# Kernel tuning notes

Hardware: AMD Instinct MI355X
Metric: run time of the kernel (lower is better)

## Reference

```python
import jax, jax.numpy as jnp
import numpy as np
import math

D_MODEL = 256
NUM_HEADS = 8
D_HEAD = 32
K_EIG = 32
NUM_BANDS = 3


def setup_inputs() -> dict:
    key = jax.random.key(0)
    ks = jax.random.split(key, 12)
    B, N = 2, 50000
    x = jax.random.normal(ks[0], (B, N, D_MODEL), dtype=jnp.float32)
    eigenvectors = jax.random.normal(ks[1], (N, K_EIG), dtype=jnp.float32) / np.sqrt(N)
    eigenvalues = jnp.sort(jax.random.uniform(ks[2], (K_EIG,), dtype=jnp.float32))
    s = 1.0 / np.sqrt(D_MODEL)
    Wq = jax.random.normal(ks[3], (NUM_HEADS * D_HEAD, D_MODEL), dtype=jnp.float32) * s
    bq = jnp.zeros((NUM_HEADS * D_HEAD,), dtype=jnp.float32)
    Wk = jax.random.normal(ks[4], (NUM_HEADS * D_HEAD, D_MODEL), dtype=jnp.float32) * s
    bk = jnp.zeros((NUM_HEADS * D_HEAD,), dtype=jnp.float32)
    Wv = jax.random.normal(ks[5], (NUM_HEADS * D_HEAD, D_MODEL), dtype=jnp.float32) * s
    bv = jnp.zeros((NUM_HEADS * D_HEAD,), dtype=jnp.float32)
    # per-head SpectralFilter params
    band_boundaries = jnp.tile(jnp.linspace(0.0, 1.0, NUM_BANDS + 1, dtype=jnp.float32)[None, :], (NUM_HEADS, 1))
    filter_weights = jnp.ones((NUM_HEADS, NUM_BANDS, K_EIG), dtype=jnp.float32) + 0.1 * jax.random.normal(ks[6], (NUM_HEADS, NUM_BANDS, K_EIG), dtype=jnp.float32)
    return {"x": x, "eigenvectors": eigenvectors, "eigenvalues": eigenvalues,
            "Wq": Wq, "bq": bq, "Wk": Wk, "bk": bk, "Wv": Wv, "bv": bv,
            "band_boundaries": band_boundaries, "filter_weights": filter_weights}


def _filter_responses(eigenvalues, band_boundaries, filter_weights):
    # eigenvalues [K]; band_boundaries [H, NB+1]; filter_weights [H, NB, K] -> [H, K]
    lam = (eigenvalues - eigenvalues.min()) / (eigenvalues.max() - eigenvalues.min() + 1e-8)  # [K]
    resp = jnp.zeros(filter_weights.shape[::2], dtype=eigenvalues.dtype)  # [H, K]
    for i in range(NUM_BANDS):  # small fixed loop; later bands overwrite (faithful to torch)
        lo = band_boundaries[:, i:i + 1]   # [H,1]
        hi = band_boundaries[:, i + 1:i + 2]
        mask = (lam[None, :] >= lo) & (lam[None, :] < hi)  # [H,K]
        resp = jnp.where(mask, filter_weights[:, i, :], resp)
    return resp


def reference(x, eigenvectors, eigenvalues, Wq, bq, Wk, bk, Wv, bv, band_boundaries, filter_weights):
    B, N, D = x.shape
    H, Dh = NUM_HEADS, D_HEAD
    Q = (x @ Wq.T + bq).reshape(B, N, H, Dh)
    K = (x @ Wk.T + bk).reshape(B, N, H, Dh)
    V = (x @ Wv.T + bv).reshape(B, N, H, Dh)
    # project to spectral domain: [B,K,H,Dh]
    Qf = jnp.einsum('nk,bnhd->bkhd', eigenvectors, Q)
    Kf = jnp.einsum('nk,bnhd->bkhd', eigenvectors, K)
    Vf = jnp.einsum('nk,bnhd->bkhd', eigenvectors, V)
    resp = _filter_responses(eigenvalues, band_boundaries, filter_weights)  # [H,K]
    g = resp.T[None, :, :, None]  # [1,K,H,1]
    Qf, Kf, Vf = Qf * g, Kf * g, Vf * g
    scores = jnp.einsum('bkhd,blhd->bkhl', Qf, Kf) / math.sqrt(Dh)  # [B,K,H,K]
    attn = jax.nn.softmax(scores, axis=-1)
    out_freq = jnp.einsum('bkhl,blhd->bkhd', attn, Vf)
    out = jnp.einsum('nk,bkhd->bnhd', eigenvectors, out_freq)
    return out.reshape(B, N, H * Dh)
```

## Files before the change

kernel.cpp:

```cpp
#include <hip/hip_runtime.h>
#include <hip/hip_bf16.h>


constexpr int D = 256;

__global__ __launch_bounds__(256) void k_colsum(const float* __restrict__ E,
                                                float* __restrict__ pS, int N) {
  int k = threadIdx.x & 31;
  int rg = threadIdx.x >> 5;
  int rs = (N + 255) >> 8;
  int n0 = blockIdx.x * rs;
  int n1 = n0 + rs; if (n1 > N) n1 = N;
  float acc = 0.f;
  for (int n = n0 + rg; n < n1; n += 8) acc += E[(size_t)n * 32 + k];
  __shared__ float red[256];
  red[threadIdx.x] = acc;
  __syncthreads();
  if (threadIdx.x < 32) {
    float t = red[threadIdx.x];
#pragma unroll
    for (int i = 1; i < 8; ++i) t += red[i * 32 + threadIdx.x];
    pS[blockIdx.x * 32 + threadIdx.x] = t;
  }
}

__global__ __launch_bounds__(256) void k_partial(const float* __restrict__ x,
                                                 const float* __restrict__ E,
                                                 float* __restrict__ pU,
                                                 int N, int nchunk, int rpc) {
  int blk = blockIdx.x;
  int c = blk % nchunk;
  int b = blk / nchunk;
  int t = threadIdx.x;
  int w = t >> 6;
  int lane = t & 63;
  int n0 = c * rpc;
  int n1 = n0 + rpc; if (n1 > N) n1 = N;
  int nrows = n1 - n0;

  float4 a0 = {0,0,0,0}, a1 = {0,0,0,0}, a2 = {0,0,0,0}, a3 = {0,0,0,0};
  float4 a4 = {0,0,0,0}, a5 = {0,0,0,0}, a6 = {0,0,0,0}, a7 = {0,0,0,0};

  __shared__ __align__(16) float Elds[200 * 32];

  if (nrows > 0) {
    {
      const float4* Esrc = reinterpret_cast<const float4*>(E + (size_t)n0 * 32);
      float4* Edst = reinterpret_cast<float4*>(Elds);
      int nf4 = nrows * 8;
      for (int i = t; i < nf4; i += 256) Edst[i] = Esrc[i];
    }
    __syncthreads();

    const float* xb = x + (size_t)b * N * D + 4 * lane;
#define XLD(r) (*reinterpret_cast<const float4*>(xb + (size_t)(n0 + (r)) * D))
#define XLDC(r) XLD((r) < nrows ? (r) : nrows - 1)

    float4 p0 = XLDC(0), p1 = XLDC(1), p2 = XLDC(2), p3 = XLDC(3);
    float4 p4 = XLDC(4), p5 = XLDC(5), p6 = XLDC(6), p7 = XLDC(7);

#define FMAROW(eA, eB, xq)                                                     \
  a0.x=fmaf(eA.x,xq.x,a0.x); a0.y=fmaf(eA.x,xq.y,a0.y);                        \
  a0.z=fmaf(eA.x,xq.z,a0.z); a0.w=fmaf(eA.x,xq.w,a0.w);                        \
  a1.x=fmaf(eA.y,xq.x,a1.x); a1.y=fmaf(eA.y,xq.y,a1.y);                        \
  a1.z=fmaf(eA.y,xq.z,a1.z); a1.w=fmaf(eA.y,xq.w,a1.w);                        \
  a2.x=fmaf(eA.z,xq.x,a2.x); a2.y=fmaf(eA.z,xq.y,a2.y);                        \
  a2.z=fmaf(eA.z,xq.z,a2.z); a2.w=fmaf(eA.z,xq.w,a2.w);                        \
  a3.x=fmaf(eA.w,xq.x,a3.x); a3.y=fmaf(eA.w,xq.y,a3.y);                        \
  a3.z=fmaf(eA.w,xq.z,a3.z); a3.w=fmaf(eA.w,xq.w,a3.w);                        \
  a4.x=fmaf(eB.x,xq.x,a4.x); a4.y=fmaf(eB.x,xq.y,a4.y);                        \
  a4.z=fmaf(eB.x,xq.z,a4.z); a4.w=fmaf(eB.x,xq.w,a4.w);                        \
  a5.x=fmaf(eB.y,xq.x,a5.x); a5.y=fmaf(eB.y,xq.y,a5.y);                        \
  a5.z=fmaf(eB.y,xq.z,a5.z); a5.w=fmaf(eB.y,xq.w,a5.w);                        \
  a6.x=fmaf(eB.z,xq.x,a6.x); a6.y=fmaf(eB.z,xq.y,a6.y);                        \
  a6.z=fmaf(eB.z,xq.z,a6.z); a6.w=fmaf(eB.z,xq.w,a6.w);                        \
  a7.x=fmaf(eB.w,xq.x,a7.x); a7.y=fmaf(eB.w,xq.y,a7.y);                        \
  a7.z=fmaf(eB.w,xq.z,a7.z); a7.w=fmaf(eB.w,xq.w,a7.w);

#define ROW4(base, q0, q1, q2, q3) {                                           \
    const float* eb = Elds + (base) * 32 + 8 * w;                              \
    float4 eA0 = *(const float4*)(eb);      float4 eB0 = *(const float4*)(eb+4);   \
    float4 eA1 = *(const float4*)(eb+32);   float4 eB1 = *(const float4*)(eb+36);  \
    float4 eA2 = *(const float4*)(eb+64);   float4 eB2 = *(const float4*)(eb+68);  \
    float4 eA3 = *(const float4*)(eb+96);   float4 eB3 = *(const float4*)(eb+100); \
    FMAROW(eA0, eB0, q0) FMAROW(eA1, eB1, q1)                                  \
    FMAROW(eA2, eB2, q2) FMAROW(eA3, eB3, q3) }

#define ROW1(r, q) {                                                           \
    const float* eb = Elds + (r) * 32 + 8 * w;                                 \
    float4 eA = *(const float4*)(eb); float4 eB = *(const float4*)(eb + 4);    \
    FMAROW(eA, eB, q) }

    int i = 0;
#pragma unroll 1
    for (; i + 8 <= nrows; i += 8) {
      ROW4(i, p0, p1, p2, p3)
      p0 = XLDC(i + 8);  p1 = XLDC(i + 9);  p2 = XLDC(i + 10); p3 = XLDC(i + 11);
      ROW4(i + 4, p4, p5, p6, p7)
      p4 = XLDC(i + 12); p5 = XLDC(i + 13); p6 = XLDC(i + 14); p7 = XLDC(i + 15);
    }
    int rem = nrows - i;
    if (rem > 0) ROW1(i + 0, p0)
    if (rem > 1) ROW1(i + 1, p1)
    if (rem > 2) ROW1(i + 2, p2)
    if (rem > 3) ROW1(i + 3, p3)
    if (rem > 4) ROW1(i + 4, p4)
    if (rem > 5) ROW1(i + 5, p5)
    if (rem > 6) ROW1(i + 6, p6)
#undef ROW1
#undef ROW4
#undef FMAROW
#undef XLDC
#undef XLD
  }

  float* o = pU + (size_t)blk * 8192 + (size_t)(8 * w) * 256 + 4 * lane;
  *reinterpret_cast<float4*>(o + 0 * 256) = a0;
  *reinterpret_cast<float4*>(o + 1 * 256) = a1;
  *reinterpret_cast<float4*>(o + 2 * 256) = a2;
  *reinterpret_cast<float4*>(o + 3 * 256) = a3;
  *reinterpret_cast<float4*>(o + 4 * 256) = a4;
  *reinterpret_cast<float4*>(o + 5 * 256) = a5;
  *reinterpret_cast<float4*>(o + 6 * 256) = a6;
  *reinterpret_cast<float4*>(o + 7 * 256) = a7;
}

__global__ __launch_bounds__(256) void k_reduce(const float* __restrict__ pU,
                                                float* __restrict__ U, int nchunk) {
  int e = blockIdx.x * 32 + (threadIdx.x & 31);
  int sub = threadIdx.x >> 5;
  int b = e >> 13;
  int kd = e & 8191;
  const float* p = pU + (size_t)b * nchunk * 8192 + kd;
  float a0 = 0.f, a1 = 0.f, a2 = 0.f, a3 = 0.f;
  int c = sub;
#pragma unroll 1
  for (; c + 24 < nchunk; c += 32) {
    a0 += p[(size_t)c * 8192];
    a1 += p[(size_t)(c + 8) * 8192];
    a2 += p[(size_t)(c + 16) * 8192];
    a3 += p[(size_t)(c + 24) * 8192];
  }
  for (; c < nchunk; c += 8) a0 += p[(size_t)c * 8192];
  __shared__ float red[256];
  red[threadIdx.x] = (a0 + a1) + (a2 + a3);
  __syncthreads();
  if (threadIdx.x < 32) {
    float s = red[threadIdx.x];
#pragma unroll
    for (int i = 1; i < 8; ++i) s += red[i * 32 + threadIdx.x];
    U[e] = s;
  }
}

__global__ __launch_bounds__(256) void k_project(
    const float* __restrict__ U, const float* __restrict__ pS,
    const float* __restrict__ Wq, const float* __restrict__ bq,
    const float* __restrict__ Wk, const float* __restrict__ bk,
    const float* __restrict__ Wv, const float* __restrict__ bv,
    const float* __restrict__ ev, const float* __restrict__ bb,
    const float* __restrict__ fw,
    float* __restrict__ Qfg, float* __restrict__ Kfg, float* __restrict__ Vfg) {
  int blk = blockIdx.x;
  int k = blk & 31;
  int t = threadIdx.x;
  __shared__ __align__(16) float u[256];
  __shared__ float red[256];
  u[t] = U[(size_t)blk * 256 + t];
  red[t] = pS[t * 32 + k];
  __syncthreads();
#pragma unroll
  for (int off = 128; off > 0; off >>= 1) {
    if (t < off) red[t] += red[t + off];
    __syncthreads();
  }
  float sk = red[0];

  float mnf = ev[0], mxf = ev[0];
#pragma unroll
  for (int i = 1; i < 32; ++i) { float v = ev[i]; mnf = fminf(mnf, v); mxf = fmaxf(mxf, v); }
  double mn = (double)mnf, mx = (double)mxf;
  double lam = ((double)ev[k] - mn) / (mx - mn + 1e-8);
  int h = t >> 5;
  float g = 0.f;
#pragma unroll
  for (int i = 0; i < 3; ++i) {
    double lo = (double)bb[h * 4 + i], hi = (double)bb[h * 4 + i + 1];
    if (lam >= lo && lam < hi) g = fw[(h * 3 + i) * 32 + k];
  }

  const float4* u4 = reinterpret_cast<const float4*>(u);
  const float4* wq4 = reinterpret_cast<const float4*>(Wq) + (size_t)t * 64;
  const float4* wk4 = reinterpret_cast<const float4*>(Wk) + (size_t)t * 64;
  const float4* wv4 = reinterpret_cast<const float4*>(Wv) + (size_t)t * 64;
  float aq = 0.f, ak = 0.f, av = 0.f;
#pragma unroll 4
  for (int j = 0; j < 64; ++j) {
    float4 uv = u4[j];
    float4 q = wq4[j], kk = wk4[j], vv = wv4[j];
    aq = fmaf(uv.x, q.x, aq);  aq = fmaf(uv.y, q.y, aq);
    aq = fmaf(uv.z, q.z, aq);  aq = fmaf(uv.w, q.w, aq);
    ak = fmaf(uv.x, kk.x, ak); ak = fmaf(uv.y, kk.y, ak);
    ak = fmaf(uv.z, kk.z, ak); ak = fmaf(uv.w, kk.w, ak);
    av = fmaf(uv.x, vv.x, av); av = fmaf(uv.y, vv.y, av);
    av = fmaf(uv.z, vv.z, av); av = fmaf(uv.w, vv.w, av);
  }
  Qfg[(size_t)blk * 256 + t] = (aq + bq[t] * sk) * g;
  Kfg[(size_t)blk * 256 + t] = (ak + bk[t] * sk) * g;
  Vfg[(size_t)blk * 256 + t] = (av + bv[t] * sk) * g;
}

__global__ __launch_bounds__(1024) void k_attn(const float* __restrict__ Qfg,
                                               const float* __restrict__ Kfg,
                                               const float* __restrict__ Vfg,
                                               float* __restrict__ of) {
  int blk = blockIdx.x;
  int b = blk >> 3, h = blk & 7;
  int tid = threadIdx.x;
  int row = tid >> 5, col = tid & 31;
  __shared__ float Q[32][33], Kt[32][33], V[32][33], A[32][33];
  size_t base = (size_t)b * 32 * 256 + h * 32;
  Q[row][col]  = Qfg[base + row * 256 + col];
  Kt[row][col] = Kfg[base + row * 256 + col];
  V[row][col]  = Vfg[base + row * 256 + col];
  __syncthreads();
  float sc = 0.f;
#pragma unroll
  for (int d0 = 0; d0 < 32; ++d0) sc = fmaf(Q[row][d0], Kt[col][d0], sc);
  sc *= 0.17677669529663687f;
  float m = sc;
#pragma unroll
  for (int o = 16; o > 0; o >>= 1) m = fmaxf(m, __shfl_xor(m, o, 32));
  float p = expf(sc - m);
  float su = p;
#pragma unroll
  for (int o = 16; o > 0; o >>= 1) su += __shfl_xor(su, o, 32);
  A[row][col] = p / su;
  __syncthreads();
  float o_ = 0.f;
#pragma unroll
  for (int l = 0; l < 32; ++l) o_ = fmaf(A[row][l], V[l][col], o_);
  of[base + row * 256 + col] = o_;
}

__global__ __launch_bounds__(256) void k_expand(const float* __restrict__ E,
                                                const float* __restrict__ of,
                                                float* __restrict__ out,
                                                int N, int rows) {
  int n0 = blockIdx.x * rows;
  int n1 = n0 + rows; if (n1 > N) n1 = N;
  int nrows = n1 - n0;
  if (nrows <= 0) return;
  int t = threadIdx.x;

  const float* ofb = of + t;
#define LDF(i) float2 f##i = make_float2(ofb[(i) * 256], ofb[8192 + (i) * 256]);
  LDF(0)  LDF(1)  LDF(2)  LDF(3)  LDF(4)  LDF(5)  LDF(6)  LDF(7)
  LDF(8)  LDF(9)  LDF(10) LDF(11) LDF(12) LDF(13) LDF(14) LDF(15)
  LDF(16) LDF(17) LDF(18) LDF(19) LDF(20) LDF(21) LDF(22) LDF(23)
  LDF(24) LDF(25) LDF(26) LDF(27) LDF(28) LDF(29) LDF(30) LDF(31)
#undef LDF

  __shared__ __align__(16) float Elds[50 * 32];
  {
    const float4* Esrc = reinterpret_cast<const float4*>(E + (size_t)n0 * 32);
    float4* Edst = reinterpret_cast<float4*>(Elds);
    int nf4 = nrows * 8;
    for (int i = t; i < nf4; i += 256) Edst[i] = Esrc[i];
  }
  __syncthreads();

  float* o0 = out + t;
  float* o1 = out + (size_t)N * D + t;

#define EXP2(s, fk) { acc0 = fmaf(s, fk.x, acc0); acc1 = fmaf(s, fk.y, acc1); }
#pragma unroll 1
  for (int i = 0; i < nrows; ++i) {
    const float4* er = reinterpret_cast<const float4*>(Elds + i * 32);
    float4 e0 = er[0], e1 = er[1], e2 = er[2], e3 = er[3];
    float4 e4 = er[4], e5 = er[5], e6 = er[6], e7 = er[7];
    float acc0 = 0.f, acc1 = 0.f;
    EXP2(e0.x, f0)  EXP2(e0.y, f1)  EXP2(e0.z, f2)  EXP2(e0.w, f3)
    EXP2(e1.x, f4)  EXP2(e1.y, f5)  EXP2(e1.z, f6)  EXP2(e1.w, f7)
    EXP2(e2.x, f8)  EXP2(e2.y, f9)  EXP2(e2.z, f10) EXP2(e2.w, f11)
    EXP2(e3.x, f12) EXP2(e3.y, f13) EXP2(e3.z, f14) EXP2(e3.w, f15)
    EXP2(e4.x, f16) EXP2(e4.y, f17) EXP2(e4.z, f18) EXP2(e4.w, f19)
    EXP2(e5.x, f20) EXP2(e5.y, f21) EXP2(e5.z, f22) EXP2(e5.w, f23)
    EXP2(e6.x, f24) EXP2(e6.y, f25) EXP2(e6.z, f26) EXP2(e6.w, f27)
    EXP2(e7.x, f28) EXP2(e7.y, f29) EXP2(e7.z, f30) EXP2(e7.w, f31)
    size_t roff = (size_t)(n0 + i) * D;
    o0[roff] = acc0;
    o1[roff] = acc1;
  }
#undef EXP2
}

extern "C" void kernel_launch(void* const* d_in, const int* in_sizes, int n_in,
                              void* d_out, int out_size, void* d_ws, size_t ws_size,
                              hipStream_t stream) {
  const float* x  = (const float*)d_in[0];
  const float* E  = (const float*)d_in[1];
  const float* ev = (const float*)d_in[2];
  const float* Wq = (const float*)d_in[3];
  const float* bq = (const float*)d_in[4];
  const float* Wk = (const float*)d_in[5];
  const float* bk = (const float*)d_in[6];
  const float* Wv = (const float*)d_in[7];
  const float* bv = (const float*)d_in[8];
  const float* bb = (const float*)d_in[9];
  const float* fw = (const float*)d_in[10];
  float* out = (float*)d_out;
  float* ws  = (float*)d_ws;

  const int N = in_sizes[1] / 32;
  const int B = in_sizes[0] / (N * 256);

  float* U   = ws;
  float* Qfg = ws + 16384;
  float* Kfg = ws + 32768;
  float* Vfg = ws + 49152;
  float* of  = ws + 65536;
  float* pS  = ws + 81920;
  float* pU  = ws + 90112;

  int nchunk = 512;
  if ((90112 + (size_t)B * nchunk * 8192) * sizeof(float) > ws_size) nchunk = 256;
  int rpc = (N + nchunk - 1) / nchunk;

  k_colsum<<<256, 256, 0, stream>>>(E, pS, N);
  k_partial<<<B * nchunk, 256, 0, stream>>>(x, E, pU, N, nchunk, rpc);
  k_reduce<<<B * 8192 / 32, 256, 0, stream>>>(pU, U, nchunk);
  k_project<<<B * 32, 256, 0, stream>>>(U, pS, Wq, bq, Wk, bk, Wv, bv,
                                        ev, bb, fw, Qfg, Kfg, Vfg);
  k_attn<<<B * 8, 1024, 0, stream>>>(Qfg, Kfg, Vfg, of);
  int rows = 50;
  int nbr = (N + rows - 1) / rows;
  k_expand<<<nbr, 256, 0, stream>>>(E, of, out, N, rows);
}
```

Measured before the change: 118.0 us.

## Split k_partial over d-halves and row-interleave waves with LDS reduction

After: 248.5 us. 111% more time.

```diff
diff --git a/kernel.cpp b/kernel.cpp
--- a/kernel.cpp
+++ b/kernel.cpp
@@ -24,105 +24,112 @@
   }
 }
 
-__global__ __launch_bounds__(256) void k_partial(const float* __restrict__ x,
-                                                 const float* __restrict__ E,
-                                                 float* __restrict__ pU,
-                                                 int N, int nchunk, int rpc) {
+__global__ __launch_bounds__(256, 4) void k_partial(const float* __restrict__ x,
+                                                    const float* __restrict__ E,
+                                                    float* __restrict__ pU,
+                                                    int N, int nchunk, int rpc) {
   int blk = blockIdx.x;
-  int c = blk % nchunk;
-  int b = blk / nchunk;
+  int dh = blk & 1;
+  int bc = blk >> 1;
+  int c = bc % nchunk;
+  int b = bc / nchunk;
   int t = threadIdx.x;
-  int w = t >> 6;
+  int ro = t >> 6;
   int lane = t & 63;
   int n0 = c * rpc;
   int n1 = n0 + rpc; if (n1 > N) n1 = N;
-  int nrows = n1 - n0;
-
-  float4 a0 = {0,0,0,0}, a1 = {0,0,0,0}, a2 = {0,0,0,0}, a3 = {0,0,0,0};
-  float4 a4 = {0,0,0,0}, a5 = {0,0,0,0}, a6 = {0,0,0,0}, a7 = {0,0,0,0};
-
-  __shared__ __align__(16) float Elds[200 * 32];
+  int nrows = n1 - n0; if (nrows < 0) nrows = 0;
+
+  __shared__ __align__(16) float smem[4096];
 
   if (nrows > 0) {
-    {
-      const float4* Esrc = reinterpret_cast<const float4*>(E + (size_t)n0 * 32);
-      float4* Edst = reinterpret_cast<float4*>(Elds);
-      int nf4 = nrows * 8;
-      for (int i = t; i < nf4; i += 256) Edst[i] = Esrc[i];
+    const float4* Esrc = reinterpret_cast<const float4*>(E + (size_t)n0 * 32);
+    float4* Edst = reinterpret_cast<float4*>(smem);
+    int nf4 = nrows * 8;
+    for (int i = t; i < nf4; i += 256) Edst[i] = Esrc[i];
+  }
+  __syncthreads();
+
+  float2 a0={0,0},a1={0,0},a2={0,0},a3={0,0},a4={0,0},a5={0,0},a6={0,0},a7={0,0};
+  float2 a8={0,0},a9={0,0},a10={0,0},a11={0,0},a12={0,0},a13={0,0},a14={0,0},a15={0,0};
+  float2 a16={0,0},a17={0,0},a18={0,0},a19={0,0},a20={0,0},a21={0,0},a22={0,0},a23={0,0};
+  float2 a24={0,0},a25={0,0},a26={0,0},a27={0,0},a28={0,0},a29={0,0},a30={0,0},a31={0,0};
+
+  int mrows = (nrows > ro) ? ((nrows - ro + 3) >> 2) : 0;
+
+  if (mrows > 0) {
+    const float* xb = x + (size_t)b * N * D + dh * 128 + 2 * lane;
+#define XLD(j) (*reinterpret_cast<const float2*>( \
+    xb + (size_t)(n0 + ro + 4 * ((j) < mrows ? (j) : mrows - 1)) * D))
+
+    float2 p0 = XLD(0), p1 = XLD(1), p2 = XLD(2), p3 = XLD(3);
+    float2 p4 = XLD(4), p5 = XLD(5), p6 = XLD(6), p7 = XLD(7);
+
+#define FMAK(e, aA, aB, aC, aD)                                   \
+  aA.x = fmaf(e.x, xq.x, aA.x); aA.y = fmaf(e.x, xq.y, aA.y);     \
+  aB.x = fmaf(e.y, xq.x, aB.x); aB.y = fmaf(e.y, xq.y, aB.y);     \
+  aC.x = fmaf(e.z, xq.x, aC.x); aC.y = fmaf(e.z, xq.y, aC.y);     \
+  aD.x = fmaf(e.w, xq.x, aD.x); aD.y = fmaf(e.w, xq.y, aD.y);
+
+#define ROW1(j, q) {                                              \
+    const float4* eb = reinterpret_cast<const float4*>(           \
+        smem + (ro + 4 * (j)) * 32);                              \
+    float4 e0 = eb[0], e1 = eb[1], e2 = eb[2], e3 = eb[3];        \
+    float4 e4 = eb[4], e5 = eb[5], e6 = eb[6], e7 = eb[7];        \
+    float2 xq = q;                                                \
+    FMAK(e0, a0,  a1,  a2,  a3)  FMAK(e1, a4,  a5,  a6,  a7)      \
+    FMAK(e2, a8,  a9,  a10, a11) FMAK(e3, a12, a13, a14, a15)     \
+    FMAK(e4, a16, a17, a18, a19) FMAK(e5, a20, a21, a22, a23)     \
+    FMAK(e6, a24, a25, a26, a27) FMAK(e7, a28, a29, a30, a31) }
+
+    int j = 0;
+#pragma unroll 1
+    for (; j + 8 <= mrows; j += 8) {
+      ROW1(j + 0, p0) ROW1(j + 1, p1) ROW1(j + 2, p2) ROW1(j + 3, p3)
+      p0 = XLD(j + 8);  p1 = XLD(j + 9);  p2 = XLD(j + 10); p3 = XLD(j + 11);
+      ROW1(j + 4, p4) ROW1(j + 5, p5) ROW1(j + 6, p6) ROW1(j + 7, p7)
+      p4 = XLD(j + 12); p5 = XLD(j + 13); p6 = XLD(j + 14); p7 = XLD(j + 15);
     }
-    __syncthreads();
-
-    const float* xb = x + (size_t)b * N * D + 4 * lane;
-#define XLD(r) (*reinterpret_cast<const float4*>(xb + (size_t)(n0 + (r)) * D))
-#define XLDC(r) XLD((r) < nrows ? (r) : nrows - 1)
-
-    float4 p0 = XLDC(0), p1 = XLDC(1), p2 = XLDC(2), p3 = XLDC(3);
-    float4 p4 = XLDC(4), p5 = XLDC(5), p6 = XLDC(6), p7 = XLDC(7);
-
-#define FMAROW(eA, eB, xq)                                                     \
-  a0.x=fmaf(eA.x,xq.x,a0.x); a0.y=fmaf(eA.x,xq.y,a0.y);                        \
-  a0.z=fmaf(eA.x,xq.z,a0.z); a0.w=fmaf(eA.x,xq.w,a0.w);                        \
-  a1.x=fmaf(eA.y,xq.x,a1.x); a1.y=fmaf(eA.y,xq.y,a1.y);                        \
-  a1.z=fmaf(eA.y,xq.z,a1.z); a1.w=fmaf(eA.y,xq.w,a1.w);                        \
-  a2.x=fmaf(eA.z,xq.x,a2.x); a2.y=fmaf(eA.z,xq.y,a2.y);                        \
-  a2.z=fmaf(eA.z,xq.z,a2.z); a2.w=fmaf(eA.z,xq.w,a2.w);                        \
-  a3.x=fmaf(eA.w,xq.x,a3.x); a3.y=fmaf(eA.w,xq.y,a3.y);                        \
-  a3.z=fmaf(eA.w,xq.z,a3.z); a3.w=fmaf(eA.w,xq.w,a3.w);                        \
-  a4.x=fmaf(eB.x,xq.x,a4.x); a4.y=fmaf(eB.x,xq.y,a4.y);                        \
-  a4.z=fmaf(eB.x,xq.z,a4.z); a4.w=fmaf(eB.x,xq.w,a4.w);                        \
-  a5.x=fmaf(eB.y,xq.x,a5.x); a5.y=fmaf(eB.y,xq.y,a5.y);                        \
-  a5.z=fmaf(eB.y,xq.z,a5.z); a5.w=fmaf(eB.y,xq.w,a5.w);                        \
-  a6.x=fmaf(eB.z,xq.x,a6.x); a6.y=fmaf(eB.z,xq.y,a6.y);                        \
-  a6.z=fmaf(eB.z,xq.z,a6.z); a6.w=fmaf(eB.z,xq.w,a6.w);                        \
-  a7.x=fmaf(eB.w,xq.x,a7.x); a7.y=fmaf(eB.w,xq.y,a7.y);                        \
-  a7.z=fmaf(eB.w,xq.z,a7.z); a7.w=fmaf(eB.w,xq.w,a7.w);
-
-#define ROW4(base, q0, q1, q2, q3) {                                           \
-    const float* eb = Elds + (base) * 32 + 8 * w;                              \
-    float4 eA0 = *(const float4*)(eb);      float4 eB0 = *(const float4*)(eb+4);   \
-    float4 eA1 = *(const float4*)(eb+32);   float4 eB1 = *(const float4*)(eb+36);  \
-    float4 eA2 = *(const float4*)(eb+64);   float4 eB2 = *(const float4*)(eb+68);  \
-    float4 eA3 = *(const float4*)(eb+96);   float4 eB3 = *(const float4*)(eb+100); \
-    FMAROW(eA0, eB0, q0) FMAROW(eA1, eB1, q1)                                  \
-    FMAROW(eA2, eB2, q2) FMAROW(eA3, eB3, q3) }
-
-#define ROW1(r, q) {                                                           \
-    const float* eb = Elds + (r) * 32 + 8 * w;                                 \
-    float4 eA = *(const float4*)(eb); float4 eB = *(const float4*)(eb + 4);    \
-    FMAROW(eA, eB, q) }
-
-    int i = 0;
-#pragma unroll 1
-    for (; i + 8 <= nrows; i += 8) {
-      ROW4(i, p0, p1, p2, p3)
-      p0 = XLDC(i + 8);  p1 = XLDC(i + 9);  p2 = XLDC(i + 10); p3 = XLDC(i + 11);
-      ROW4(i + 4, p4, p5, p6, p7)
-      p4 = XLDC(i + 12); p5 = XLDC(i + 13); p6 = XLDC(i + 14); p7 = XLDC(i + 15);
-    }
-    int rem = nrows - i;
-    if (rem > 0) ROW1(i + 0, p0)
-    if (rem > 1) ROW1(i + 1, p1)
-    if (rem > 2) ROW1(i + 2, p2)
-    if (rem > 3) ROW1(i + 3, p3)
-    if (rem > 4) ROW1(i + 4, p4)
-    if (rem > 5) ROW1(i + 5, p5)
-    if (rem > 6) ROW1(i + 6, p6)
+    int rem = mrows - j;
+    if (rem > 0) ROW1(j + 0, p0)
+    if (rem > 1) ROW1(j + 1, p1)
+    if (rem > 2) ROW1(j + 2, p2)
+    if (rem > 3) ROW1(j + 3, p3)
+    if (rem > 4) ROW1(j + 4, p4)
+    if (rem > 5) ROW1(j + 5, p5)
+    if (rem > 6) ROW1(j + 6, p6)
 #undef ROW1
-#undef ROW4
-#undef FMAROW
-#undef XLDC
+#undef FMAK
 #undef XLD
   }
 
-  float* o = pU + (size_t)blk * 8192 + (size_t)(8 * w) * 256 + 4 * lane;
-  *reinterpret_cast<float4*>(o + 0 * 256) = a0;
-  *reinterpret_cast<float4*>(o + 1 * 256) = a1;
-  *reinterpret_cast<float4*>(o + 2 * 256) = a2;
-  *reinterpret_cast<float4*>(o + 3 * 256) = a3;
-  *reinterpret_cast<float4*>(o + 4 * 256) = a4;
-  *reinterpret_cast<float4*>(o + 5 * 256) = a5;
-  *reinterpret_cast<float4*>(o + 6 * 256) = a6;
-  *reinterpret_cast<float4*>(o + 7 * 256) = a7;
+  float2* rb = reinterpret_cast<float2*>(smem);
+  float* o = pU + ((size_t)bc * 2 + dh) * 4096;
+
+#define OCT(g, cA, cB, cC, cD, cE, cF, cG, cH)                    \
+  __syncthreads();                                                \
+  rb[(ro * 8 + 0) * 64 + lane] = cA; rb[(ro * 8 + 1) * 64 + lane] = cB; \
+  rb[(ro * 8 + 2) * 64 + lane] = cC; rb[(ro * 8 + 3) * 64 + lane] = cD; \
+  rb[(ro * 8 + 4) * 64 + lane] = cE; rb[(ro * 8 + 5) * 64 + lane] = cF; \
+  rb[(ro * 8 + 6) * 64 + lane] = cG; rb[(ro * 8 + 7) * 64 + lane] = cH; \
+  __syncthreads();                                                \
+  _Pragma("unroll")                                               \
+  for (int i = 0; i < 2; ++i) {                                   \
+    int idx = i * 256 + t;                                        \
+    int kk = idx >> 6, ll = idx & 63;                             \
+    float2 s0 = rb[(0 * 8 + kk) * 64 + ll], s1 = rb[(1 * 8 + kk) * 64 + ll]; \
+    float2 s2 = rb[(2 * 8 + kk) * 64 + ll], s3 = rb[(3 * 8 + kk) * 64 + ll]; \
+    float2 sv;                                                    \
+    sv.x = (s0.x + s1.x) + (s2.x + s3.x);                         \
+    sv.y = (s0.y + s1.y) + (s2.y + s3.y);                         \
+    *reinterpret_cast<float2*>(o + ((g) * 8 + kk) * 128 + 2 * ll) = sv; \
+  }
+
+  OCT(0, a0,  a1,  a2,  a3,  a4,  a5,  a6,  a7)
+  OCT(1, a8,  a9,  a10, a11, a12, a13, a14, a15)
+  OCT(2, a16, a17, a18, a19, a20, a21, a22, a23)
+  OCT(3, a24, a25, a26, a27, a28, a29, a30, a31)
+#undef OCT
 }
 
 __global__ __launch_bounds__(256) void k_reduce(const float* __restrict__ pU,
@@ -131,7 +138,10 @@
   int sub = threadIdx.x >> 5;
   int b = e >> 13;
   int kd = e & 8191;
-  const float* p = pU + (size_t)b * nchunk * 8192 + kd;
+  int k = kd >> 8;
+  int d = kd & 255;
+  int dh = d >> 7, dl = d & 127;
+  const float* p = pU + (size_t)b * nchunk * 8192 + (size_t)dh * 4096 + k * 128 + dl;
   float a0 = 0.f, a1 = 0.f, a2 = 0.f, a3 = 0.f;
   int c = sub;
 #pragma unroll 1
@@ -328,7 +338,7 @@
   int rpc = (N + nchunk - 1) / nchunk;
 
   k_colsum<<<256, 256, 0, stream>>>(E, pS, N);
-  k_partial<<<B * nchunk, 256, 0, stream>>>(x, E, pU, N, nchunk, rpc);
+  k_partial<<<B * nchunk * 2, 256, 0, stream>>>(x, E, pU, N, nchunk, rpc);
   k_reduce<<<B * 8192 / 32, 256, 0, stream>>>(pU, U, nchunk);
   k_project<<<B * 32, 256, 0, stream>>>(U, pS, Wq, bq, Wk, bk, Wv, bv,
                                         ev, bb, fw, Qfg, Kfg, Vfg);
```
